# Kernel tuning notes

Hardware: AMD Instinct MI355X
Metric: run time of the kernel (lower is better)

## Reference

```python
import jax, jax.numpy as jnp
import numpy as np

EPS = 1e-7          # keras.backend.epsilon()
L2_EPS = 1e-12      # tf.math.l2_normalize epsilon


def _l2_normalize(v):
    # tf.math.l2_normalize: v * rsqrt(max(sum(v^2), 1e-12))
    sq = jnp.sum(v * v, axis=-1, keepdims=True)
    return v * jax.lax.rsqrt(jnp.maximum(sq, L2_EPS))


def setup_inputs() -> dict:
    key = jax.random.key(0)
    k1, k2 = jax.random.split(key)
    x = jax.random.normal(k1, (4, 2048, 1024), dtype=jnp.float32)
    ref = jax.random.normal(k2, (8192, 1024), dtype=jnp.float32)
    return {"x": x, "ref": ref}


def reference(x, ref):
    # inputs += K.epsilon()
    xn = _l2_normalize(x + EPS)          # [B, N, D]
    refn = _l2_normalize(ref)            # [M, D]
    # fused form of sum(xn[..., N, 1, D] * refn[1, M, D], axis=-1) -> [B, N, M]
    return jnp.einsum('bnd,md->bnm', xn, refn)
```

## Files before the change

### kernel.cpp

```cpp
#include <hip/hip_runtime.h>
#include <hip/hip_bf16.h>
#include <stdint.h>

typedef __bf16 bf16x8 __attribute__((ext_vector_type(8)));
typedef float f32x4 __attribute__((ext_vector_type(4)));

#define GLB_AS __attribute__((address_space(1)))
#define LDS_AS __attribute__((address_space(3)))

__device__ __forceinline__ void gload_lds16(const void* g, void* l) {
    __builtin_amdgcn_global_load_lds((GLB_AS void*)(g), (LDS_AS void*)(l), 16, 0, 0);
}

#define GM 8192
#define GN 8192
#define GK 1024

__global__ __launch_bounds__(256) void normalize_rows(
    const float* __restrict__ x, const float* __restrict__ ref,
    __bf16* __restrict__ outA, __bf16* __restrict__ outB)
{
    const int row = blockIdx.x;
    const bool isX = row < 8192;
    const size_t r = isX ? (size_t)row : (size_t)(row - 8192);
    const float* src = isX ? (x + r * 1024) : (ref + r * 1024);
    __bf16* dst = isX ? (outA + r * 1024) : (outB + r * 1024);
    const float eps = isX ? 1e-7f : 0.0f;

    const int t = threadIdx.x;
    float4 v = reinterpret_cast<const float4*>(src)[t];
    v.x += eps; v.y += eps; v.z += eps; v.w += eps;
    float ss = v.x * v.x + v.y * v.y + v.z * v.z + v.w * v.w;

    #pragma unroll
    for (int o = 32; o; o >>= 1) ss += __shfl_xor(ss, o, 64);

    __shared__ float red[4];
    const int wv = t >> 6, lane = t & 63;
    if (lane == 0) red[wv] = ss;
    __syncthreads();
    const float tot = red[0] + red[1] + red[2] + red[3];
    const float inv = rsqrtf(fmaxf(tot, 1e-12f));

    __bf16 b[4];
    b[0] = (__bf16)(v.x * inv);
    b[1] = (__bf16)(v.y * inv);
    b[2] = (__bf16)(v.z * inv);
    b[3] = (__bf16)(v.w * inv);
    uint2 pk;
    __builtin_memcpy(&pk, b, 8);
    reinterpret_cast<uint2*>(dst)[t] = pk;
}

__global__ __launch_bounds__(512, 2) void gemm_pers(
    const __bf16* __restrict__ A, const __bf16* __restrict__ B,
    float* __restrict__ C)
{
    __shared__ __bf16 As[2][2][128][64];
    __shared__ __bf16 Bs[2][2][128][64];

    const int bid = blockIdx.x;
    const int xcd = bid & 7, sq = bid >> 3;
    const int u = (xcd & 3) * 4 + (sq & 3);
    const int v = (xcd >> 2) * 8 + (sq >> 2);
    const size_t u0 = (size_t)u * 512;
    const size_t v0 = (size_t)v * 512;

    const int tid  = threadIdx.x;
    const int wave = tid >> 6;
    const int lane = tid & 63;
    const int wr = wave >> 2;
    const int wc = wave & 3;

    const int srow  = lane >> 3;
    const int sslot = (lane & 7) ^ srow;
    const int fr = lane & 15;
    const int fs = lane >> 4;

    bf16x8 af[4][2];
    bf16x8 bq[2][2][2];
    f32x4  acc[8][4] = {};

#define BASE_M(q) (u0 + ((((q) >> 4) == 1 || ((q) >> 4) == 2) ? 256 : 0))
#define BASE_N(q) (v0 + ((((q) >> 4) >= 2) ? 256 : 0))

#define STAGE_A(rM, q, h, b) { \
    const size_t kcol = (size_t)((q) & 15) * 64; \
    _Pragma("unroll") \
    for (int j = 0; j < 2; ++j) { \
        const size_t grow = (rM) + (size_t)(j) * 128 + (h) * 64 + wave * 8 + srow; \
        const char* src = (const char*)A + (grow * GK + kcol) * 2 + sslot * 16; \
        char* dst = (char*)&As[b][h][0][0] + (j * 64 + wave * 8) * 128; \
        gload_lds16(src, dst); } }

#define STAGE_B(rN, q, h, b) { \
    const size_t kcol = (size_t)((q) & 15) * 64; \
    _Pragma("unroll") \
    for (int j = 0; j < 2; ++j) { \
        const int l = j * 64 + wave * 8 + srow; \
        const size_t grow = (rN) + (size_t)(l >> 5) * 64 + (h) * 32 + (l & 31); \
        const char* src = (const char*)B + (grow * GK + kcol) * 2 + sslot * 16; \
        char* dst = (char*)&Bs[b][h][0][0] + (j * 64 + wave * 8) * 128; \
        gload_lds16(src, dst); } }

#define LDA(qm, b) { \
    _Pragma("unroll") \
    for (int m = 0; m < 4; ++m) { \
        const int l = wr * 64 + m * 16 + fr; \
        _Pragma("unroll") \
        for (int ks = 0; ks < 2; ++ks) { \
            const int slot = (ks * 4 + fs) ^ (l & 7); \
            af[m][ks] = *(const bf16x8*)((const char*)&As[b][qm][0][0] + l * 128 + slot * 16); } } }

#define LDB(qn, b) { \
    _Pragma("unroll") \
    for (int n = 0; n < 2; ++n) { \
        const int l = wc * 32 + n * 16 + fr; \
        _Pragma("unroll") \
        for (int ks = 0; ks < 2; ++ks) { \
            const int slot = (ks * 4 + fs) ^ (l & 7); \
            bq[qn][n][ks] = *(const bf16x8*)((const char*)&Bs[b][qn][0][0] + l * 128 + slot * 16); } } }

#define QMFMA(qm, qn) { \
    __builtin_amdgcn_s_setprio(1); \
    _Pragma("unroll") \
    for (int ks = 0; ks < 2; ++ks) \
    _Pragma("unroll") \
    for (int m = 0; m < 4; ++m) \
    _Pragma("unroll") \
    for (int n = 0; n < 2; ++n) \
        acc[(qm) * 4 + m][(qn) * 2 + n] = __builtin_amdgcn_mfma_f32_16x16x32_bf16( \
            bq[qn][n][ks], af[m][ks], acc[(qm) * 4 + m][(qn) * 2 + n], 0, 0, 0); \
    __builtin_amdgcn_s_setprio(0); }

#define QMFMA_F(qm, qn) { \
    __builtin_amdgcn_s_setprio(1); \
    _Pragma("unroll") \
    for (int m = 0; m < 4; ++m) \
    _Pragma("unroll") \
    for (int n = 0; n < 2; ++n) \
        acc[(qm) * 4 + m][(qn) * 2 + n] = __builtin_amdgcn_mfma_f32_16x16x32_bf16( \
            bq[qn][n][0], af[m][0], (f32x4){0.f, 0.f, 0.f, 0.f}, 0, 0, 0); \
    _Pragma("unroll") \
    for (int m = 0; m < 4; ++m) \
    _Pragma("unroll") \
    for (int n = 0; n < 2; ++n) \
        acc[(qm) * 4 + m][(qn) * 2 + n] = __builtin_amdgcn_mfma_f32_16x16x32_bf16( \
            bq[qn][n][1], af[m][1], acc[(qm) * 4 + m][(qn) * 2 + n], 0, 0, 0); \
    __builtin_amdgcn_s_setprio(0); }

#define STORE_QUAD(qm, qn, rM, rN) { \
    _Pragma("unroll") \
    for (int m = 0; m < 4; ++m) \
    _Pragma("unroll") \
    for (int n = 0; n < 2; ++n) { \
        const size_t row = (rM) + (size_t)wr * 128 + (qm) * 64 + m * 16 + (lane & 15); \
        const size_t col = (rN) + (size_t)wc * 64 + (qn) * 32 + n * 16 + (lane >> 4) * 4; \
        *reinterpret_cast<f32x4*>(&C[row * (size_t)GN + col]) = acc[(qm) * 4 + m][(qn) * 2 + n]; } }

#define BAR() __builtin_amdgcn_s_barrier()
#define WAIT_LGKM0() { asm volatile("s_waitcnt lgkmcnt(0)" ::: "memory"); __builtin_amdgcn_sched_barrier(0); }
#define WAIT_VM(n)   { asm volatile("s_waitcnt vmcnt(" #n ")" ::: "memory"); __builtin_amdgcn_sched_barrier(0); }

    STAGE_A(u0, 0, 0, 0); STAGE_A(u0, 0, 1, 0); STAGE_B(v0, 0, 0, 0); STAGE_B(v0, 0, 1, 0);
    STAGE_A(u0, 1, 0, 1); STAGE_B(v0, 1, 0, 1); STAGE_B(v0, 1, 1, 1);
    WAIT_VM(6);
    BAR();

    #pragma unroll 1
    for (int i = 0; i < 32; ++i) {
        const int q1 = 2 * i + 1, q2 = 2 * i + 2, q3 = 2 * i + 3;
        const bool more  = (i < 31);
        const bool first = (i & 7) == 0;
        const bool lastt = (i & 7) == 7;
        const int  tj = i >> 3;
        const size_t rMs = u0 + ((tj == 1 || tj == 2) ? 256 : 0);
        const size_t rNs = v0 + ((tj >= 2) ? 256 : 0);
        const size_t rM2 = BASE_M(q2), rN2 = BASE_N(q2);
        const size_t rM3 = BASE_M(q3), rN3 = BASE_N(q3);

        LDA(0, 0); LDB(0, 0);
        STAGE_A(rMs, q1, 1, 1);
        BAR(); WAIT_LGKM0();
        if (first) { QMFMA_F(0, 0); } else { QMFMA(0, 0); }
        BAR();
        LDB(1, 0);
        if (more) STAGE_A(rM2, q2, 0, 0);
        BAR(); WAIT_LGKM0();
        if (first) { QMFMA_F(0, 1); } else { QMFMA(0, 1); }
        BAR();
        LDA(1, 0);
        if (more) STAGE_B(rN2, q2, 0, 0);
        BAR(); WAIT_LGKM0();
        if (first) { QMFMA_F(1, 0); } else { QMFMA(1, 0); }
        BAR();
        if (more) { STAGE_B(rN2, q2, 1, 0); WAIT_VM(6); }
        else      { WAIT_VM(0); }
        BAR();
        if (first) { QMFMA_F(1, 1); } else { QMFMA(1, 1); }
        BAR();
        LDA(0, 1); LDB(0, 1);
        if (more) STAGE_A(rM2, q2, 1, 0);
        BAR(); WAIT_LGKM0();
        QMFMA(0, 0);
        if (lastt) STORE_QUAD(0, 0, rMs, rNs);
        BAR();
        LDB(1, 1);
        if (more) STAGE_A(rM3, q3, 0, 1);
        BAR(); WAIT_LGKM0();
        QMFMA(0, 1);
        if (lastt) STORE_QUAD(0, 1, rMs, rNs);
        BAR();
        LDA(1, 1);
        if (more) STAGE_B(rN3, q3, 0, 1);
        BAR(); WAIT_LGKM0();
        QMFMA(1, 0);
        if (lastt) STORE_QUAD(1, 0, rMs, rNs);
        BAR();
        if (more) {
            STAGE_B(rN3, q3, 1, 1);
            if (lastt) { WAIT_VM(38); } else { WAIT_VM(6); }
            BAR();
            QMFMA(1, 1);
            if (lastt) STORE_QUAD(1, 1, rMs, rNs);
            BAR();
        } else {
            BAR();
            QMFMA(1, 1);
            STORE_QUAD(1, 1, rMs, rNs);
        }
    }

#undef BASE_M
#undef BASE_N
#undef STAGE_A
#undef STAGE_B
#undef LDA
#undef LDB
#undef QMFMA
#undef QMFMA_F
#undef STORE_QUAD
#undef BAR
#undef WAIT_LGKM0
#undef WAIT_VM
}

__global__ __launch_bounds__(256) void naive_pairwise(
    const float* __restrict__ x, const float* __restrict__ ref,
    float* __restrict__ out)
{
    const int row = blockIdx.x >> 5;
    const int j = (blockIdx.x & 31) * 256 + threadIdx.x;
    const float* xr = x + (size_t)row * 1024;
    const float* rr = ref + (size_t)j * 1024;

    __shared__ float xs[1024];
    float part = 0.f;
    for (int k = threadIdx.x; k < 1024; k += 256) {
        float v = xr[k] + 1e-7f;
        xs[k] = v;
        part += v * v;
    }
    #pragma unroll
    for (int o = 32; o; o >>= 1) part += __shfl_xor(part, o, 64);
    __shared__ float red[4];
    if ((threadIdx.x & 63) == 0) red[threadIdx.x >> 6] = part;
    __syncthreads();
    const float ssx = red[0] + red[1] + red[2] + red[3];

    float ssr = 0.f, dot = 0.f;
    for (int k = 0; k < 1024; ++k) {
        float r = rr[k];
        ssr += r * r;
        dot += r * xs[k];
    }
    out[(size_t)row * 8192 + j] =
        dot * rsqrtf(fmaxf(ssx, 1e-12f)) * rsqrtf(fmaxf(ssr, 1e-12f));
}

extern "C" void kernel_launch(void* const* d_in, const int* in_sizes, int n_in,
                              void* d_out, int out_size, void* d_ws, size_t ws_size,
                              hipStream_t stream) {
    const float* x   = (const float*)d_in[0];
    const float* ref = (const float*)d_in[1];
    float* out = (float*)d_out;

    const size_t need = (size_t)GM * GK * sizeof(__bf16) * 2;
    if (ws_size >= need) {
        __bf16* wsA = (__bf16*)d_ws;
        __bf16* wsB = wsA + (size_t)GM * GK;
        normalize_rows<<<16384, 256, 0, stream>>>(x, ref, wsA, wsB);
        gemm_pers<<<256, 512, 0, stream>>>(wsA, wsB, out);
    } else {
        naive_pairwise<<<8192 * 32, 256, 0, stream>>>(x, ref, out);
    }
}
```

Measured before the change: 183.5 us.

## Overlap LDS fragment loads with MFMA phases and halve barriers in GEMM loop

Restructures the persistent bf16 GEMM main loop so the LDS-to-register fragment loads for the next quadrant are issued right after the current quadrant's MFMAs, ahead of a single barrier per phase. The loop drops the explicit lgkmcnt(0) waits and the paired barriers around each MFMA block. The first fragment load is hoisted before the loop and the last phase prefetches the next iteration's fragments. This targets barrier and LDS latency stalls, but relies on compiler-inserted waits for correctness and raises register pressure from the live prefetched fragments.

```diff
diff --git a/kernel.cpp b/kernel.cpp
--- a/kernel.cpp
+++ b/kernel.cpp
@@ -52,7 +52,7 @@
     reinterpret_cast<uint2*>(dst)[t] = pk;
 }
 
-__global__ __launch_bounds__(512, 2) void gemm_pers(
+__global__ __launch_bounds__(512, 2) void gemm_pipe(
     const __bf16* __restrict__ A, const __bf16* __restrict__ B,
     float* __restrict__ C)
 {
@@ -149,6 +149,8 @@
             bq[qn][n][1], af[m][1], acc[(qm) * 4 + m][(qn) * 2 + n], 0, 0, 0); \
     __builtin_amdgcn_s_setprio(0); }
 
+#define MFMA_PH(isf, qm, qn) { if (isf) { QMFMA_F(qm, qn); } else { QMFMA(qm, qn); } }
+
 #define STORE_QUAD(qm, qn, rM, rN) { \
     _Pragma("unroll") \
     for (int m = 0; m < 4; ++m) \
@@ -158,14 +160,14 @@
         const size_t col = (rN) + (size_t)wc * 64 + (qn) * 32 + n * 16 + (lane >> 4) * 4; \
         *reinterpret_cast<f32x4*>(&C[row * (size_t)GN + col]) = acc[(qm) * 4 + m][(qn) * 2 + n]; } }
 
-#define BAR() __builtin_amdgcn_s_barrier()
-#define WAIT_LGKM0() { asm volatile("s_waitcnt lgkmcnt(0)" ::: "memory"); __builtin_amdgcn_sched_barrier(0); }
+#define BARS() { __builtin_amdgcn_sched_barrier(0); __builtin_amdgcn_s_barrier(); }
 #define WAIT_VM(n)   { asm volatile("s_waitcnt vmcnt(" #n ")" ::: "memory"); __builtin_amdgcn_sched_barrier(0); }
 
     STAGE_A(u0, 0, 0, 0); STAGE_A(u0, 0, 1, 0); STAGE_B(v0, 0, 0, 0); STAGE_B(v0, 0, 1, 0);
     STAGE_A(u0, 1, 0, 1); STAGE_B(v0, 1, 0, 1); STAGE_B(v0, 1, 1, 1);
     WAIT_VM(6);
-    BAR();
+    BARS();
+    LDA(0, 0); LDB(0, 0);
 
     #pragma unroll 1
     for (int i = 0; i < 32; ++i) {
@@ -173,59 +175,49 @@
         const bool more  = (i < 31);
         const bool first = (i & 7) == 0;
         const bool lastt = (i & 7) == 7;
-        const int  tj = i >> 3;
-        const size_t rMs = u0 + ((tj == 1 || tj == 2) ? 256 : 0);
-        const size_t rNs = v0 + ((tj >= 2) ? 256 : 0);
+        const size_t rMs = u0 + (((i >> 3) == 1 || (i >> 3) == 2) ? 256 : 0);
+        const size_t rNs = v0 + (((i >> 3) >= 2) ? 256 : 0);
         const size_t rM2 = BASE_M(q2), rN2 = BASE_N(q2);
         const size_t rM3 = BASE_M(q3), rN3 = BASE_N(q3);
 
-        LDA(0, 0); LDB(0, 0);
         STAGE_A(rMs, q1, 1, 1);
-        BAR(); WAIT_LGKM0();
-        if (first) { QMFMA_F(0, 0); } else { QMFMA(0, 0); }
-        BAR();
+        MFMA_PH(first, 0, 0);
         LDB(1, 0);
+        BARS();
         if (more) STAGE_A(rM2, q2, 0, 0);
-        BAR(); WAIT_LGKM0();
-        if (first) { QMFMA_F(0, 1); } else { QMFMA(0, 1); }
-        BAR();
+        MFMA_PH(first, 0, 1);
         LDA(1, 0);
+        BARS();
         if (more) STAGE_B(rN2, q2, 0, 0);
-        BAR(); WAIT_LGKM0();
-        if (first) { QMFMA_F(1, 0); } else { QMFMA(1, 0); }
-        BAR();
+        MFMA_PH(first, 1, 0);
+        BARS();
         if (more) { STAGE_B(rN2, q2, 1, 0); WAIT_VM(6); }
         else      { WAIT_VM(0); }
-        BAR();
-        if (first) { QMFMA_F(1, 1); } else { QMFMA(1, 1); }
-        BAR();
+        MFMA_PH(first, 1, 1);
         LDA(0, 1); LDB(0, 1);
+        BARS();
         if (more) STAGE_A(rM2, q2, 1, 0);
-        BAR(); WAIT_LGKM0();
         QMFMA(0, 0);
+        LDB(1, 1);
         if (lastt) STORE_QUAD(0, 0, rMs, rNs);
-        BAR();
-        LDB(1, 1);
+        BARS();
         if (more) STAGE_A(rM3, q3, 0, 1);
-        BAR(); WAIT_LGKM0();
         QMFMA(0, 1);
+        LDA(1, 1);
         if (lastt) STORE_QUAD(0, 1, rMs, rNs);
-        BAR();
-        LDA(1, 1);
+        BARS();
         if (more) STAGE_B(rN3, q3, 0, 1);
-        BAR(); WAIT_LGKM0();
         QMFMA(1, 0);
         if (lastt) STORE_QUAD(1, 0, rMs, rNs);
-        BAR();
+        BARS();
         if (more) {
             STAGE_B(rN3, q3, 1, 1);
-            if (lastt) { WAIT_VM(38); } else { WAIT_VM(6); }
-            BAR();
+            if (lastt) { WAIT_VM(30); } else { WAIT_VM(6); }
             QMFMA(1, 1);
+            LDA(0, 0); LDB(0, 0);
             if (lastt) STORE_QUAD(1, 1, rMs, rNs);
-            BAR();
+            BARS();
         } else {
-            BAR();
             QMFMA(1, 1);
             STORE_QUAD(1, 1, rMs, rNs);
         }
@@ -239,9 +231,9 @@
 #undef LDB
 #undef QMFMA
 #undef QMFMA_F
+#undef MFMA_PH
 #undef STORE_QUAD
-#undef BAR
-#undef WAIT_LGKM0
+#undef BARS
 #undef WAIT_VM
 }
 
@@ -290,7 +282,7 @@
         __bf16* wsA = (__bf16*)d_ws;
         __bf16* wsB = wsA + (size_t)GM * GK;
         normalize_rows<<<16384, 256, 0, stream>>>(x, ref, wsA, wsB);
-        gemm_pers<<<256, 512, 0, stream>>>(wsA, wsB, out);
+        gemm_pipe<<<256, 512, 0, stream>>>(wsA, wsB, out);
     } else {
         naive_pairwise<<<8192 * 32, 256, 0, stream>>>(x, ref, out);
     }
```

Result: slower. 519.7 us (+183.2%).

## Switch GEMM to 32x32x16 MFMA with new LDS swizzle and stage schedule

Applied to the files above, without the earlier changes.

Replaces the 16x16x32 bf16 MFMA tiling with 32x32x16 MFMA using 16-wide accumulators. The LDS fragment loads and the XOR swizzle (now also keyed on wave and the row's upper bits) are reworked to match. The per-iteration schedule drops from eight to four compute phases with fewer barriers and regrouped global->LDS staging. The aim is fewer LDS reads per FLOP and less barrier overhead. The risks are changed vmcnt waits that could race, and a store pattern with less coalesced rows.

```diff
diff --git a/kernel.cpp b/kernel.cpp
--- a/kernel.cpp
+++ b/kernel.cpp
@@ -4,6 +4,7 @@
 
 typedef __bf16 bf16x8 __attribute__((ext_vector_type(8)));
 typedef float f32x4 __attribute__((ext_vector_type(4)));
+typedef float f32x16 __attribute__((ext_vector_type(16)));
 
 #define GLB_AS __attribute__((address_space(1)))
 #define LDS_AS __attribute__((address_space(3)))
@@ -52,7 +53,7 @@
     reinterpret_cast<uint2*>(dst)[t] = pk;
 }
 
-__global__ __launch_bounds__(512, 2) void gemm_pers(
+__global__ __launch_bounds__(512, 2) void gemm_p4(
     const __bf16* __restrict__ A, const __bf16* __restrict__ B,
     float* __restrict__ C)
 {
@@ -73,13 +74,14 @@
     const int wc = wave & 3;
 
     const int srow  = lane >> 3;
-    const int sslot = (lane & 7) ^ srow;
-    const int fr = lane & 15;
-    const int fs = lane >> 4;
-
-    bf16x8 af[4][2];
-    bf16x8 bq[2][2][2];
-    f32x4  acc[8][4] = {};
+    const int sslot = (lane & 7) ^ srow ^ wave;
+    const int l31 = lane & 31;
+    const int hi  = lane >> 5;
+
+    bf16x8 af[2][4];
+    bf16x8 bq[2][4];
+    f32x16 acc[4][2];
+    const f32x16 ZV = {};
 
 #define BASE_M(q) (u0 + ((((q) >> 4) == 1 || ((q) >> 4) == 2) ? 256 : 0))
 #define BASE_N(q) (v0 + ((((q) >> 4) >= 2) ? 256 : 0))
@@ -103,60 +105,67 @@
         char* dst = (char*)&Bs[b][h][0][0] + (j * 64 + wave * 8) * 128; \
         gload_lds16(src, dst); } }
 
-#define LDA(qm, b) { \
-    _Pragma("unroll") \
-    for (int m = 0; m < 4; ++m) { \
-        const int l = wr * 64 + m * 16 + fr; \
-        _Pragma("unroll") \
-        for (int ks = 0; ks < 2; ++ks) { \
-            const int slot = (ks * 4 + fs) ^ (l & 7); \
-            af[m][ks] = *(const bf16x8*)((const char*)&As[b][qm][0][0] + l * 128 + slot * 16); } } }
-
-#define LDB(qn, b) { \
-    _Pragma("unroll") \
-    for (int n = 0; n < 2; ++n) { \
-        const int l = wc * 32 + n * 16 + fr; \
-        _Pragma("unroll") \
-        for (int ks = 0; ks < 2; ++ks) { \
-            const int slot = (ks * 4 + fs) ^ (l & 7); \
-            bq[qn][n][ks] = *(const bf16x8*)((const char*)&Bs[b][qn][0][0] + l * 128 + slot * 16); } } }
-
-#define QMFMA(qm, qn) { \
+#define LDA32(qm, b) { \
+    _Pragma("unroll") \
+    for (int msl = 0; msl < 2; ++msl) { \
+        const int r = wr * 64 + msl * 32 + l31; \
+        const int rs = (r & 7) ^ ((r >> 3) & 7); \
+        _Pragma("unroll") \
+        for (int kk = 0; kk < 4; ++kk) { \
+            const int slot = (kk * 2 + hi) ^ rs; \
+            af[msl][kk] = *(const bf16x8*)((const char*)&As[b][qm][0][0] + r * 128 + slot * 16); } } }
+
+#define LDB32(b) { \
+    const int rb_ = wc * 32 + l31; \
+    const int rsb_ = (rb_ & 7) ^ ((rb_ >> 3) & 7); \
+    _Pragma("unroll") \
+    for (int ns = 0; ns < 2; ++ns) { \
+        _Pragma("unroll") \
+        for (int kk = 0; kk < 4; ++kk) { \
+            const int slot = (kk * 2 + hi) ^ rsb_; \
+            bq[ns][kk] = *(const bf16x8*)((const char*)&Bs[b][ns][0][0] + rb_ * 128 + slot * 16); } } }
+
+#define MFMAQ(isf, qm) { \
     __builtin_amdgcn_s_setprio(1); \
-    _Pragma("unroll") \
-    for (int ks = 0; ks < 2; ++ks) \
-    _Pragma("unroll") \
-    for (int m = 0; m < 4; ++m) \
-    _Pragma("unroll") \
-    for (int n = 0; n < 2; ++n) \
-        acc[(qm) * 4 + m][(qn) * 2 + n] = __builtin_amdgcn_mfma_f32_16x16x32_bf16( \
-            bq[qn][n][ks], af[m][ks], acc[(qm) * 4 + m][(qn) * 2 + n], 0, 0, 0); \
+    if (isf) { \
+        _Pragma("unroll") \
+        for (int msl = 0; msl < 2; ++msl) \
+        _Pragma("unroll") \
+        for (int ns = 0; ns < 2; ++ns) \
+            acc[(qm) * 2 + msl][ns] = __builtin_amdgcn_mfma_f32_32x32x16_bf16( \
+                bq[ns][0], af[msl][0], ZV, 0, 0, 0); \
+    } else { \
+        _Pragma("unroll") \
+        for (int msl = 0; msl < 2; ++msl) \
+        _Pragma("unroll") \
+        for (int ns = 0; ns < 2; ++ns) \
+            acc[(qm) * 2 + msl][ns] = __builtin_amdgcn_mfma_f32_32x32x16_bf16( \
+                bq[ns][0], af[msl][0], acc[(qm) * 2 + msl][ns], 0, 0, 0); \
+    } \
+    _Pragma("unroll") \
+    for (int kk = 1; kk < 4; ++kk) \
+    _Pragma("unroll") \
+    for (int msl = 0; msl < 2; ++msl) \
+    _Pragma("unroll") \
+    for (int ns = 0; ns < 2; ++ns) \
+        acc[(qm) * 2 + msl][ns] = __builtin_amdgcn_mfma_f32_32x32x16_bf16( \
+            bq[ns][kk], af[msl][kk], acc[(qm) * 2 + msl][ns], 0, 0, 0); \
     __builtin_amdgcn_s_setprio(0); }
 
-#define QMFMA_F(qm, qn) { \
-    __builtin_amdgcn_s_setprio(1); \
-    _Pragma("unroll") \
-    for (int m = 0; m < 4; ++m) \
-    _Pragma("unroll") \
-    for (int n = 0; n < 2; ++n) \
-        acc[(qm) * 4 + m][(qn) * 2 + n] = __builtin_amdgcn_mfma_f32_16x16x32_bf16( \
-            bq[qn][n][0], af[m][0], (f32x4){0.f, 0.f, 0.f, 0.f}, 0, 0, 0); \
-    _Pragma("unroll") \
-    for (int m = 0; m < 4; ++m) \
-    _Pragma("unroll") \
-    for (int n = 0; n < 2; ++n) \
-        acc[(qm) * 4 + m][(qn) * 2 + n] = __builtin_amdgcn_mfma_f32_16x16x32_bf16( \
-            bq[qn][n][1], af[m][1], acc[(qm) * 4 + m][(qn) * 2 + n], 0, 0, 0); \
-    __builtin_amdgcn_s_setprio(0); }
-
-#define STORE_QUAD(qm, qn, rM, rN) { \
-    _Pragma("unroll") \
-    for (int m = 0; m < 4; ++m) \
-    _Pragma("unroll") \
-    for (int n = 0; n < 2; ++n) { \
-        const size_t row = (rM) + (size_t)wr * 128 + (qm) * 64 + m * 16 + (lane & 15); \
-        const size_t col = (rN) + (size_t)wc * 64 + (qn) * 32 + n * 16 + (lane >> 4) * 4; \
-        *reinterpret_cast<f32x4*>(&C[row * (size_t)GN + col]) = acc[(qm) * 4 + m][(qn) * 2 + n]; } }
+#define STORE2(qm, rM, rN) { \
+    _Pragma("unroll") \
+    for (int msl = 0; msl < 2; ++msl) \
+    _Pragma("unroll") \
+    for (int ns = 0; ns < 2; ++ns) { \
+        const size_t row = (rM) + (size_t)wr * 128 + ((qm) * 2 + msl) * 32 + l31; \
+        _Pragma("unroll") \
+        for (int qd = 0; qd < 4; ++qd) { \
+            const size_t col = (rN) + (size_t)wc * 64 + ns * 32 + qd * 8 + hi * 4; \
+            f32x4 v_ = { acc[(qm) * 2 + msl][ns][qd * 4 + 0], \
+                         acc[(qm) * 2 + msl][ns][qd * 4 + 1], \
+                         acc[(qm) * 2 + msl][ns][qd * 4 + 2], \
+                         acc[(qm) * 2 + msl][ns][qd * 4 + 3] }; \
+            *reinterpret_cast<f32x4*>(&C[row * (size_t)GN + col]) = v_; } } }
 
 #define BAR() __builtin_amdgcn_s_barrier()
 #define WAIT_LGKM0() { asm volatile("s_waitcnt lgkmcnt(0)" ::: "memory"); __builtin_amdgcn_sched_barrier(0); }
@@ -173,61 +182,43 @@
         const bool more  = (i < 31);
         const bool first = (i & 7) == 0;
         const bool lastt = (i & 7) == 7;
-        const int  tj = i >> 3;
-        const size_t rMs = u0 + ((tj == 1 || tj == 2) ? 256 : 0);
-        const size_t rNs = v0 + ((tj >= 2) ? 256 : 0);
+        const size_t rMs = u0 + (((i >> 3) == 1 || (i >> 3) == 2) ? 256 : 0);
+        const size_t rNs = v0 + (((i >> 3) >= 2) ? 256 : 0);
+        const size_t rM1 = BASE_M(q1);
         const size_t rM2 = BASE_M(q2), rN2 = BASE_N(q2);
         const size_t rM3 = BASE_M(q3), rN3 = BASE_N(q3);
 
-        LDA(0, 0); LDB(0, 0);
-        STAGE_A(rMs, q1, 1, 1);
-        BAR(); WAIT_LGKM0();
-        if (first) { QMFMA_F(0, 0); } else { QMFMA(0, 0); }
+        STAGE_A(rM1, q1, 1, 1);
+        LDA32(0, 0); LDB32(0);
+        BAR(); WAIT_LGKM0();
+        MFMAQ(first, 0);
         BAR();
-        LDB(1, 0);
-        if (more) STAGE_A(rM2, q2, 0, 0);
-        BAR(); WAIT_LGKM0();
-        if (first) { QMFMA_F(0, 1); } else { QMFMA(0, 1); }
+
+        if (more) { STAGE_A(rM2, q2, 0, 0); STAGE_B(rN2, q2, 0, 0); }
+        LDA32(1, 0);
+        BAR(); WAIT_LGKM0();
+        MFMAQ(first, 1);
+        if (more) { WAIT_VM(6); } else { WAIT_VM(2); }
         BAR();
-        LDA(1, 0);
-        if (more) STAGE_B(rN2, q2, 0, 0);
-        BAR(); WAIT_LGKM0();
-        if (first) { QMFMA_F(1, 0); } else { QMFMA(1, 0); }
+
+        if (more) { STAGE_B(rN2, q2, 1, 0); STAGE_A(rM2, q2, 1, 0); }
+        LDA32(0, 1); LDB32(1);
+        BAR(); WAIT_LGKM0();
+        MFMAQ(false, 0);
+        if (lastt) STORE2(0, rMs, rNs);
+        if (more) {
+            if (lastt) { WAIT_VM(24); } else { WAIT_VM(8); }
+        } else { WAIT_VM(16); }
         BAR();
-        if (more) { STAGE_B(rN2, q2, 1, 0); WAIT_VM(6); }
-        else      { WAIT_VM(0); }
-        BAR();
-        if (first) { QMFMA_F(1, 1); } else { QMFMA(1, 1); }
-        BAR();
-        LDA(0, 1); LDB(0, 1);
-        if (more) STAGE_A(rM2, q2, 1, 0);
-        BAR(); WAIT_LGKM0();
-        QMFMA(0, 0);
-        if (lastt) STORE_QUAD(0, 0, rMs, rNs);
-        BAR();
-        LDB(1, 1);
-        if (more) STAGE_A(rM3, q3, 0, 1);
-        BAR(); WAIT_LGKM0();
-        QMFMA(0, 1);
-        if (lastt) STORE_QUAD(0, 1, rMs, rNs);
-        BAR();
-        LDA(1, 1);
-        if (more) STAGE_B(rN3, q3, 0, 1);
-        BAR(); WAIT_LGKM0();
-        QMFMA(1, 0);
-        if (lastt) STORE_QUAD(1, 0, rMs, rNs);
-        BAR();
+
+        if (more) { STAGE_A(rM3, q3, 0, 1); STAGE_B(rN3, q3, 0, 1); STAGE_B(rN3, q3, 1, 1); }
+        LDA32(1, 1);
+        BAR(); WAIT_LGKM0();
+        MFMAQ(false, 1);
+        if (lastt) STORE2(1, rMs, rNs);
         if (more) {
-            STAGE_B(rN3, q3, 1, 1);
             if (lastt) { WAIT_VM(38); } else { WAIT_VM(6); }
             BAR();
-            QMFMA(1, 1);
-            if (lastt) STORE_QUAD(1, 1, rMs, rNs);
-            BAR();
-        } else {
-            BAR();
-            QMFMA(1, 1);
-            STORE_QUAD(1, 1, rMs, rNs);
         }
     }
 
@@ -235,11 +226,10 @@
 #undef BASE_N
 #undef STAGE_A
 #undef STAGE_B
-#undef LDA
-#undef LDB
-#undef QMFMA
-#undef QMFMA_F
-#undef STORE_QUAD
+#undef LDA32
+#undef LDB32
+#undef MFMAQ
+#undef STORE2
 #undef BAR
 #undef WAIT_LGKM0
 #undef WAIT_VM
@@ -290,7 +280,7 @@
         __bf16* wsA = (__bf16*)d_ws;
         __bf16* wsB = wsA + (size_t)GM * GK;
         normalize_rows<<<16384, 256, 0, stream>>>(x, ref, wsA, wsB);
-        gemm_pers<<<256, 512, 0, stream>>>(wsA, wsB, out);
+        gemm_p4<<<256, 512, 0, stream>>>(wsA, wsB, out);
     } else {
         naive_pairwise<<<8192 * 32, 256, 0, stream>>>(x, ref, out);
     }
```

Result: slower. 193.3 us (+5.4%).
